# Optimization experiments

Measured on AMD Instinct MI355X. Metric: run time of the kernel, lower is better.

The kernel has to match this reference:

```python
import jax, jax.numpy as jnp
import numpy as np

HIDDEN = 2048
INTERMEDIATE = 8192
NUM_EXPERTS = 8
VOCAB = 100000
EXPERT_INTER = INTERMEDIATE // NUM_EXPERTS  # 1024
B, S = 4, 4096


def setup_inputs() -> dict:
    key = jax.random.key(0)
    k1, k2, k3, k4, k5 = jax.random.split(key, 5)
    hidden_states = jax.random.normal(k1, (B, S, HIDDEN), dtype=jnp.float32)
    token_ids = jax.random.randint(k2, (B, S), 0, VOCAB, dtype=jnp.int64)
    scale = 0.02
    gate_proj = jax.random.normal(k3, (NUM_EXPERTS, HIDDEN, EXPERT_INTER), dtype=jnp.float32) * scale
    up_proj = jax.random.normal(k4, (NUM_EXPERTS, HIDDEN, EXPERT_INTER), dtype=jnp.float32) * scale
    down_proj = jax.random.normal(k5, (NUM_EXPERTS, EXPERT_INTER, HIDDEN), dtype=jnp.float32) * scale
    return {
        "hidden_states": hidden_states,
        "token_ids": token_ids,
        "gate_proj": gate_proj,
        "up_proj": up_proj,
        "down_proj": down_proj,
    }


def _token_to_expert(token_ids):
    # Buffer in the torch module maps contiguous vocab buckets to experts;
    # remainder tokens go to the last expert.
    tokens_per_expert = VOCAB // NUM_EXPERTS
    ids = jnp.clip(token_ids, 0, VOCAB - 1)
    return jnp.minimum(ids // tokens_per_expert, NUM_EXPERTS - 1)


def reference(hidden_states, token_ids, gate_proj, up_proj, down_proj):
    batch, seq_len, hidden = hidden_states.shape
    expert_ids = _token_to_expert(token_ids).reshape(-1)  # [T]
    x = hidden_states.reshape(-1, hidden)  # [T, H]
    out = jnp.zeros_like(x)
    # Fixed small loop over experts (structurally distinct weight slices).
    # Masked dense compute is mathematically identical to the torch module's
    # sort -> per-expert GEMM -> scatter-back (the permutation cancels).
    for e in range(NUM_EXPERTS):
        mask = (expert_ids == e)[:, None]  # [T, 1]
        g = x @ gate_proj[e]               # [T, I_e]
        u = x @ up_proj[e]                 # [T, I_e]
        y = (jax.nn.silu(g) * u) @ down_proj[e]  # [T, H]
        out = out + jnp.where(mask, y, jnp.zeros((), dtype=y.dtype))
    return out.reshape(batch, seq_len, hidden)
```

## Files before the change

kernel.cpp:

```cpp
#include <hip/hip_runtime.h>
#include <hip/hip_bf16.h>
#include <cstdint>
#include <cstddef>

#define HIDDEN   2048
#define EINTER   1024
#define NEXP     8
#define VOCAB_SZ 100000
#define TOK_PER_EXP (VOCAB_SZ / NEXP)

typedef unsigned short u16;
typedef __attribute__((ext_vector_type(8))) short short8;
typedef __attribute__((ext_vector_type(4))) float floatx4;

__device__ __forceinline__ int expert_of(int id) {
  id = id < 0 ? 0 : (id > VOCAB_SZ - 1 ? VOCAB_SZ - 1 : id);
  int e = id / TOK_PER_EXP;
  return e > NEXP - 1 ? NEXP - 1 : e;
}

__global__ void count_kernel(const int* __restrict__ tok_ids, int* __restrict__ counts, int T) {
  int t = blockIdx.x * blockDim.x + threadIdx.x;
  if (t < T) atomicAdd(&counts[expert_of(tok_ids[t])], 1);
}

__global__ void scan_kernel(const int* __restrict__ counts, int* __restrict__ offsets,
                            int* __restrict__ cursors) {
  if (threadIdx.x == 0) {
    int s = 0;
    for (int e = 0; e < NEXP; ++e) { offsets[e] = s; cursors[e] = s; s += counts[e]; }
  }
}

__global__ void scatter_kernel(const int* __restrict__ tok_ids, int* __restrict__ cursors,
                               int* __restrict__ tok_list, int T) {
  int t = blockIdx.x * blockDim.x + threadIdx.x;
  if (t < T) {
    int e = expert_of(tok_ids[t]);
    int pos = atomicAdd(&cursors[e], 1);
    tok_list[pos] = t;
  }
}

__global__ void gather_x_kernel(const float* __restrict__ x, const int* __restrict__ tok_list,
                                u16* __restrict__ xp) {
  const int row = blockIdx.x;
  const int tok = tok_list[row];
  const float* src = x + (size_t)tok * HIDDEN;
  u16* dst = xp + (size_t)row * HIDDEN;
  const int k = threadIdx.x * 8;
  float4 a = *(const float4*)(src + k);
  float4 b = *(const float4*)(src + k + 4);
  union { uint4 u; u16 s[8]; } pk;
  const float f[8] = {a.x, a.y, a.z, a.w, b.x, b.y, b.z, b.w};
#pragma unroll
  for (int i = 0; i < 8; ++i) {
    __hip_bfloat16 h = __float2bfloat16(f[i]);
    pk.s[i] = *reinterpret_cast<u16*>(&h);
  }
  *(uint4*)(dst + k) = pk.u;
}

__global__ void transpose_cvt_kernel(const float* __restrict__ in, u16* __restrict__ outp,
                                     int R, int C) {
  __shared__ float ts[32][33];
  const size_t bo = (size_t)blockIdx.z * R * C;
  const int c0 = blockIdx.x * 32, r0 = blockIdx.y * 32;
  const int tc = threadIdx.x & 31, tr = threadIdx.x >> 5;
#pragma unroll
  for (int i = 0; i < 4; ++i) {
    int r = tr + i * 8;
    ts[r][tc] = in[bo + (size_t)(r0 + r) * C + c0 + tc];
  }
  __syncthreads();
#pragma unroll
  for (int i = 0; i < 4; ++i) {
    int c = tr + i * 8;
    __hip_bfloat16 h = __float2bfloat16(ts[tc][c]);
    outp[bo + (size_t)(c0 + c) * R + r0 + tc] = *reinterpret_cast<u16*>(&h);
  }
}

__global__ __launch_bounds__(256, 2) void gate_up_mfma(
    const u16* __restrict__ xp,
    const u16* __restrict__ Gt,
    const u16* __restrict__ Ut,
    const int* __restrict__ counts,
    const int* __restrict__ offsets,
    u16* __restrict__ act) {
  __shared__ __align__(16) u16 As[128][72];
  __shared__ __align__(16) u16 Bg[64][72];
  __shared__ __align__(16) u16 Bu[64][72];

  const int e = blockIdx.z;
  const int cnt = counts[e];
  const int row0 = blockIdx.y * 128;
  if (row0 >= cnt) return;
  const int off = offsets[e];
  const int i0 = blockIdx.x * 64;

  const int tid  = threadIdx.x;
  const int lane = tid & 63;
  const int wave = tid >> 6;
  const int quad = lane >> 4;
  const int l16  = lane & 15;

  const int arow = tid >> 3;
  const int ach  = tid & 7;

  const int wrow = (wave & 1) * 64;
  const int wcol = (wave >> 1) * 32;

  floatx4 accg[4][2], accu[4][2];
#pragma unroll
  for (int mf = 0; mf < 4; ++mf)
#pragma unroll
    for (int nf = 0; nf < 2; ++nf) {
      floatx4 z = {0.f, 0.f, 0.f, 0.f};
      accg[mf][nf] = z; accu[mf][nf] = z;
    }

  const u16* xbase = xp + (size_t)off * HIDDEN;
  const u16* gbase = Gt + ((size_t)e * EINTER + i0) * HIDDEN;
  const u16* ubase = Ut + ((size_t)e * EINTER + i0) * HIDDEN;

  for (int k0 = 0; k0 < HIDDEN; k0 += 64) {
#pragma unroll
    for (int it = 0; it < 4; ++it) {
      int r = arow + it * 32;
      int rg = row0 + r; rg = rg < cnt ? rg : cnt - 1;
      *(uint4*)&As[r][ach * 8] = *(const uint4*)(xbase + (size_t)rg * HIDDEN + k0 + ach * 8);
    }
#pragma unroll
    for (int it = 0; it < 2; ++it) {
      int n = arow + it * 32;
      *(uint4*)&Bg[n][ach * 8] = *(const uint4*)(gbase + (size_t)n * HIDDEN + k0 + ach * 8);
      *(uint4*)&Bu[n][ach * 8] = *(const uint4*)(ubase + (size_t)n * HIDDEN + k0 + ach * 8);
    }
    __syncthreads();
#pragma unroll
    for (int s = 0; s < 2; ++s) {
      short8 af[4], bgf[2], buf2[2];
#pragma unroll
      for (int mf = 0; mf < 4; ++mf)
        af[mf] = *(const short8*)&As[wrow + mf * 16 + l16][(s * 4 + quad) * 8];
#pragma unroll
      for (int nf = 0; nf < 2; ++nf) {
        bgf[nf]  = *(const short8*)&Bg[wcol + nf * 16 + l16][(s * 4 + quad) * 8];
        buf2[nf] = *(const short8*)&Bu[wcol + nf * 16 + l16][(s * 4 + quad) * 8];
      }
#pragma unroll
      for (int mf = 0; mf < 4; ++mf)
#pragma unroll
        for (int nf = 0; nf < 2; ++nf) {
          accg[mf][nf] = __builtin_amdgcn_mfma_f32_16x16x32_bf16(af[mf], bgf[nf],  accg[mf][nf], 0, 0, 0);
          accu[mf][nf] = __builtin_amdgcn_mfma_f32_16x16x32_bf16(af[mf], buf2[nf], accu[mf][nf], 0, 0, 0);
        }
    }
    __syncthreads();
  }

#pragma unroll
  for (int mf = 0; mf < 4; ++mf)
#pragma unroll
    for (int nf = 0; nf < 2; ++nf)
#pragma unroll
      for (int rg = 0; rg < 4; ++rg) {
        int r = wrow + mf * 16 + quad * 4 + rg;
        if (row0 + r < cnt) {
          float g = accg[mf][nf][rg];
          float u = accu[mf][nf][rg];
          float y = (g / (1.f + __expf(-g))) * u;
          __hip_bfloat16 h = __float2bfloat16(y);
          act[((size_t)(off + row0 + r)) * EINTER + i0 + wcol + nf * 16 + l16] =
              *reinterpret_cast<u16*>(&h);
        }
      }
}

__global__ __launch_bounds__(256, 2) void down_mfma(
    const u16* __restrict__ act,
    const u16* __restrict__ Dt,
    const int* __restrict__ counts,
    const int* __restrict__ offsets,
    const int* __restrict__ tok_list,
    float* __restrict__ out) {
  __shared__ __align__(16) u16 As[128][72];
  __shared__ __align__(16) u16 Bs[128][72];
  __shared__ int toks[128];

  const int e = blockIdx.z;
  const int cnt = counts[e];
  const int row0 = blockIdx.y * 128;
  if (row0 >= cnt) return;
  const int off = offsets[e];
  const int j0 = blockIdx.x * 128;

  const int tid  = threadIdx.x;
  const int lane = tid & 63;
  const int wave = tid >> 6;
  const int quad = lane >> 4;
  const int l16  = lane & 15;

  const int arow = tid >> 3;
  const int ach  = tid & 7;

  const int wrow = (wave & 1) * 64;
  const int wcol = (wave >> 1) * 64;

  if (tid < 128) {
    int r = row0 + tid;
    toks[tid] = tok_list[off + (r < cnt ? r : cnt - 1)];
  }

  floatx4 acc[4][4];
#pragma unroll
  for (int mf = 0; mf < 4; ++mf)
#pragma unroll
    for (int nf = 0; nf < 4; ++nf) {
      floatx4 z = {0.f, 0.f, 0.f, 0.f};
      acc[mf][nf] = z;
    }

  const u16* abase = act + (size_t)off * EINTER;
  const u16* dbase = Dt + ((size_t)e * HIDDEN + j0) * EINTER;

  for (int k0 = 0; k0 < EINTER; k0 += 64) {
#pragma unroll
    for (int it = 0; it < 4; ++it) {
      int r = arow + it * 32;
      int rg = row0 + r; rg = rg < cnt ? rg : cnt - 1;
      *(uint4*)&As[r][ach * 8] = *(const uint4*)(abase + (size_t)rg * EINTER + k0 + ach * 8);
    }
#pragma unroll
    for (int it = 0; it < 4; ++it) {
      int n = arow + it * 32;
      *(uint4*)&Bs[n][ach * 8] = *(const uint4*)(dbase + (size_t)n * EINTER + k0 + ach * 8);
    }
    __syncthreads();
#pragma unroll
    for (int s = 0; s < 2; ++s) {
      short8 af[4], bf[4];
#pragma unroll
      for (int mf = 0; mf < 4; ++mf)
        af[mf] = *(const short8*)&As[wrow + mf * 16 + l16][(s * 4 + quad) * 8];
#pragma unroll
      for (int nf = 0; nf < 4; ++nf)
        bf[nf] = *(const short8*)&Bs[wcol + nf * 16 + l16][(s * 4 + quad) * 8];
#pragma unroll
      for (int mf = 0; mf < 4; ++mf)
#pragma unroll
        for (int nf = 0; nf < 4; ++nf)
          acc[mf][nf] = __builtin_amdgcn_mfma_f32_16x16x32_bf16(af[mf], bf[nf], acc[mf][nf], 0, 0, 0);
    }
    __syncthreads();
  }

#pragma unroll
  for (int mf = 0; mf < 4; ++mf)
#pragma unroll
    for (int nf = 0; nf < 4; ++nf)
#pragma unroll
      for (int rg = 0; rg < 4; ++rg) {
        int r = wrow + mf * 16 + quad * 4 + rg;
        if (row0 + r < cnt)
          out[(size_t)toks[r] * HIDDEN + j0 + wcol + nf * 16 + l16] = acc[mf][nf][rg];
      }
}

#define TM 64
#define TN 64
#define TK 16

__global__ __launch_bounds__(256, 2) void gate_up_fp32(
    const float* __restrict__ x, const float* __restrict__ G, const float* __restrict__ U,
    const int* __restrict__ counts, const int* __restrict__ offsets,
    const int* __restrict__ tok_list, float* __restrict__ act) {
  __shared__ __align__(16) float Xs[TK][TM + 4];
  __shared__ __align__(16) float Gs[TK][TN];
  __shared__ __align__(16) float Us[TK][TN];
  __shared__ int toks[TM];
  const int e = blockIdx.z, cnt = counts[e], row0 = blockIdx.y * TM;
  if (row0 >= cnt) return;
  const int off = offsets[e], i0 = blockIdx.x * TN, tid = threadIdx.x;
  if (tid < TM) { int r = row0 + tid; toks[tid] = tok_list[off + (r < cnt ? r : 0)]; }
  __syncthreads();
  const float* Ge = G + (size_t)e * HIDDEN * EINTER + i0;
  const float* Ue = U + (size_t)e * HIDDEN * EINTER + i0;
  const int kk_ld = tid & 15, r_ld = tid >> 4, i_ld = tid & 63, k_ld = tid >> 6;
  const int tx = tid & 15, ty = tid >> 4;
  float ag[4][4] = {{0.f}}, au[4][4] = {{0.f}};
  for (int k0 = 0; k0 < HIDDEN; k0 += TK) {
#pragma unroll
    for (int rr = 0; rr < 4; ++rr) {
      int r = r_ld + rr * 16;
      Xs[kk_ld][r] = x[(size_t)toks[r] * HIDDEN + k0 + kk_ld];
    }
#pragma unroll
    for (int kk = 0; kk < 4; ++kk) {
      int k = k_ld + kk * 4;
      Gs[k][i_ld] = Ge[(size_t)(k0 + k) * EINTER + i_ld];
      Us[k][i_ld] = Ue[(size_t)(k0 + k) * EINTER + i_ld];
    }
    __syncthreads();
#pragma unroll
    for (int kk = 0; kk < TK; ++kk) {
      float4 a = *(const float4*)&Xs[kk][ty * 4];
      float4 bg = *(const float4*)&Gs[kk][tx * 4];
      float4 bu = *(const float4*)&Us[kk][tx * 4];
      const float av[4] = {a.x, a.y, a.z, a.w}, bgv[4] = {bg.x, bg.y, bg.z, bg.w},
                  buv[4] = {bu.x, bu.y, bu.z, bu.w};
#pragma unroll
      for (int i = 0; i < 4; ++i)
#pragma unroll
        for (int j = 0; j < 4; ++j) {
          ag[i][j] = fmaf(av[i], bgv[j], ag[i][j]);
          au[i][j] = fmaf(av[i], buv[j], au[i][j]);
        }
    }
    __syncthreads();
  }
#pragma unroll
  for (int i = 0; i < 4; ++i) {
    int r = row0 + ty * 4 + i;
    if (r < cnt) {
      float4 o; float* op = (float*)&o;
#pragma unroll
      for (int j = 0; j < 4; ++j) {
        float g = ag[i][j], u = au[i][j];
        op[j] = (g / (1.0f + expf(-g))) * u;
      }
      *(float4*)&act[(size_t)(off + r) * EINTER + i0 + tx * 4] = o;
    }
  }
}

__global__ __launch_bounds__(256, 2) void down_fp32(
    const float* __restrict__ act, const float* __restrict__ D,
    const int* __restrict__ counts, const int* __restrict__ offsets,
    const int* __restrict__ tok_list, float* __restrict__ out) {
  __shared__ __align__(16) float As[TK][TM + 4];
  __shared__ __align__(16) float Ds[TK][TN];
  __shared__ int toks[TM];
  const int e = blockIdx.z, cnt = counts[e], row0 = blockIdx.y * TM;
  if (row0 >= cnt) return;
  const int off = offsets[e], j0 = blockIdx.x * TN, tid = threadIdx.x;
  if (tid < TM) { int r = row0 + tid; toks[tid] = tok_list[off + (r < cnt ? r : 0)]; }
  const float* De = D + (size_t)e * EINTER * HIDDEN + j0;
  const int kk_ld = tid & 15, r_ld = tid >> 4, i_ld = tid & 63, k_ld = tid >> 6;
  const int tx = tid & 15, ty = tid >> 4;
  float acc[4][4] = {{0.f}};
  for (int k0 = 0; k0 < EINTER; k0 += TK) {
#pragma unroll
    for (int rr = 0; rr < 4; ++rr) {
      int r = r_ld + rr * 16;
      int grow = row0 + r;
      As[kk_ld][r] = act[(size_t)(off + (grow < cnt ? grow : 0)) * EINTER + k0 + kk_ld];
    }
#pragma unroll
    for (int kk = 0; kk < 4; ++kk) {
      int k = k_ld + kk * 4;
      Ds[k][i_ld] = De[(size_t)(k0 + k) * HIDDEN + i_ld];
    }
    __syncthreads();
#pragma unroll
    for (int kk = 0; kk < TK; ++kk) {
      float4 a = *(const float4*)&As[kk][ty * 4];
      float4 b = *(const float4*)&Ds[kk][tx * 4];
      const float av[4] = {a.x, a.y, a.z, a.w}, bv[4] = {b.x, b.y, b.z, b.w};
#pragma unroll
      for (int i = 0; i < 4; ++i)
#pragma unroll
        for (int j = 0; j < 4; ++j)
          acc[i][j] = fmaf(av[i], bv[j], acc[i][j]);
    }
    __syncthreads();
  }
#pragma unroll
  for (int i = 0; i < 4; ++i) {
    int r = row0 + ty * 4 + i;
    if (r < cnt) {
      float4 o = {acc[i][0], acc[i][1], acc[i][2], acc[i][3]};
      *(float4*)&out[(size_t)toks[ty * 4 + i] * HIDDEN + j0 + tx * 4] = o;
    }
  }
}

extern "C" void kernel_launch(void* const* d_in, const int* in_sizes, int n_in,
                              void* d_out, int out_size, void* d_ws, size_t ws_size,
                              hipStream_t stream) {
  const float* x       = (const float*)d_in[0];
  const int*   tok_ids = (const int*)d_in[1];
  const float* G       = (const float*)d_in[2];
  const float* U       = (const float*)d_in[3];
  const float* D       = (const float*)d_in[4];
  float* out = (float*)d_out;

  const int T = in_sizes[0] / HIDDEN;

  int* counts   = (int*)d_ws;
  int* offsets  = counts + NEXP;
  int* cursors  = offsets + NEXP;
  int* tok_list = cursors + NEXP;
  size_t hdr_bytes = (((size_t)(3 * NEXP + T) * sizeof(int)) + 255) & ~(size_t)255;

  hipMemsetAsync(counts, 0, NEXP * sizeof(int), stream);
  count_kernel<<<(T + 255) / 256, 256, 0, stream>>>(tok_ids, counts, T);
  scan_kernel<<<1, 64, 0, stream>>>(counts, offsets, cursors);
  scatter_kernel<<<(T + 255) / 256, 256, 0, stream>>>(tok_ids, cursors, tok_list, T);

  const size_t xp_bytes  = (size_t)T * HIDDEN * 2;
  const size_t w_bytes   = (size_t)NEXP * HIDDEN * EINTER * 2;
  const size_t act_bf16  = (size_t)T * EINTER * 2;
  const size_t need_bf16 = hdr_bytes + xp_bytes + 3 * w_bytes + act_bf16;

  if (ws_size >= need_bf16) {
    char* p = (char*)d_ws + hdr_bytes;
    u16* xp = (u16*)p;             p += xp_bytes;
    u16* Gt = (u16*)p;             p += w_bytes;
    u16* Ut = (u16*)p;             p += w_bytes;
    u16* Dt = (u16*)p;             p += w_bytes;
    u16* act = (u16*)p;

    gather_x_kernel<<<T, 256, 0, stream>>>(x, tok_list, xp);
    transpose_cvt_kernel<<<dim3(EINTER / 32, HIDDEN / 32, NEXP), 256, 0, stream>>>(G, Gt, HIDDEN, EINTER);
    transpose_cvt_kernel<<<dim3(EINTER / 32, HIDDEN / 32, NEXP), 256, 0, stream>>>(U, Ut, HIDDEN, EINTER);
    transpose_cvt_kernel<<<dim3(HIDDEN / 32, EINTER / 32, NEXP), 256, 0, stream>>>(D, Dt, EINTER, HIDDEN);

    dim3 g1(EINTER / 64, (T + 127) / 128, NEXP);
    gate_up_mfma<<<g1, 256, 0, stream>>>(xp, Gt, Ut, counts, offsets, act);
    dim3 g2(HIDDEN / 128, (T + 127) / 128, NEXP);
    down_mfma<<<g2, 256, 0, stream>>>(act, Dt, counts, offsets, tok_list, out);
  } else {
    float* act = (float*)((char*)d_ws + hdr_bytes);
    dim3 g1(EINTER / TN, (T + TM - 1) / TM, NEXP);
    gate_up_fp32<<<g1, 256, 0, stream>>>(x, G, U, counts, offsets, tok_list, act);
    dim3 g2(HIDDEN / TN, (T + TM - 1) / TM, NEXP);
    down_fp32<<<g2, 256, 0, stream>>>(act, D, counts, offsets, tok_list, out);
  }
}
```

Baseline: 855.5 us.

## Use direct global-to-LDS loads with XOR swizzle and widen weight transpose

Replaces register-staged global-to-shared tile copies in both MFMA GEMM kernels with global_load_lds 16-byte direct loads. The shared tiles drop their padding and use an XOR-swizzled chunk layout so fragment reads stay free of bank conflicts. The weight transpose/convert kernel moves to 64x64 tiles with float4 reads and 16-byte bf16 writes, and gate and up are handled in one launch. This cuts VGPR pressure and load instruction count in the GEMMs and improves transpose bandwidth, but relies on the direct-to-LDS path placing data exactly where the swizzle expects.

After: 740.4 us. 13.5% less time.

```diff
diff --git a/kernel.cpp b/kernel.cpp
--- a/kernel.cpp
+++ b/kernel.cpp
@@ -17,6 +17,16 @@
   id = id < 0 ? 0 : (id > VOCAB_SZ - 1 ? VOCAB_SZ - 1 : id);
   int e = id / TOK_PER_EXP;
   return e > NEXP - 1 ? NEXP - 1 : e;
+}
+
+__device__ __forceinline__ void gl16(const u16* g, u16* l) {
+  __builtin_amdgcn_global_load_lds(
+      (const __attribute__((address_space(1))) uint32_t*)g,
+      (__attribute__((address_space(3))) uint32_t*)l, 16, 0, 0);
+}
+
+__device__ __forceinline__ short8 ldfrag(const u16* base, int row, int chunk) {
+  return *(const short8*)(base + (row << 6) + (((chunk ^ (row & 7))) << 3));
 }
 
 __global__ void count_kernel(const int* __restrict__ tok_ids, int* __restrict__ counts, int T) {
@@ -61,36 +71,42 @@
   *(uint4*)(dst + k) = pk.u;
 }
 
-__global__ void transpose_cvt_kernel(const float* __restrict__ in, u16* __restrict__ outp,
-                                     int R, int C) {
-  __shared__ float ts[32][33];
-  const size_t bo = (size_t)blockIdx.z * R * C;
-  const int c0 = blockIdx.x * 32, r0 = blockIdx.y * 32;
-  const int tc = threadIdx.x & 31, tr = threadIdx.x >> 5;
-#pragma unroll
-  for (int i = 0; i < 4; ++i) {
-    int r = tr + i * 8;
-    ts[r][tc] = in[bo + (size_t)(r0 + r) * C + c0 + tc];
-  }
+__global__ void transpose_cvt64(const float* __restrict__ in0, u16* __restrict__ out0,
+                                const float* __restrict__ in1, u16* __restrict__ out1,
+                                int R, int C, int split) {
+  __shared__ float ts[64][65];
+  const int z = blockIdx.z;
+  const bool first = (z < split) || (in1 == nullptr);
+  const float* in = first ? in0 : in1;
+  u16* outp = first ? out0 : out1;
+  const int e = first ? z : z - split;
+  const size_t bo = (size_t)e * R * C;
+  const int c0 = blockIdx.x * 64, r0 = blockIdx.y * 64;
+  const int lr = threadIdx.x >> 2, lq = threadIdx.x & 3;
+#pragma unroll
+  for (int j = 0; j < 4; ++j)
+    *(float4*)&ts[lr][lq * 16 + j * 4] =
+        *(const float4*)&in[bo + (size_t)(r0 + lr) * C + c0 + lq * 16 + j * 4];
   __syncthreads();
 #pragma unroll
-  for (int i = 0; i < 4; ++i) {
-    int c = tr + i * 8;
-    __hip_bfloat16 h = __float2bfloat16(ts[tc][c]);
-    outp[bo + (size_t)(c0 + c) * R + r0 + tc] = *reinterpret_cast<u16*>(&h);
+  for (int j = 0; j < 2; ++j) {
+    union { uint4 u; u16 s[8]; } pk;
+#pragma unroll
+    for (int i = 0; i < 8; ++i) {
+      __hip_bfloat16 h = __float2bfloat16(ts[lq * 16 + j * 8 + i][lr]);
+      pk.s[i] = *reinterpret_cast<u16*>(&h);
+    }
+    *(uint4*)&outp[bo + (size_t)(c0 + lr) * R + r0 + lq * 16 + j * 8] = pk.u;
   }
 }
 
 __global__ __launch_bounds__(256, 2) void gate_up_mfma(
-    const u16* __restrict__ xp,
-    const u16* __restrict__ Gt,
-    const u16* __restrict__ Ut,
-    const int* __restrict__ counts,
-    const int* __restrict__ offsets,
+    const u16* __restrict__ xp, const u16* __restrict__ Gt, const u16* __restrict__ Ut,
+    const int* __restrict__ counts, const int* __restrict__ offsets,
     u16* __restrict__ act) {
-  __shared__ __align__(16) u16 As[128][72];
-  __shared__ __align__(16) u16 Bg[64][72];
-  __shared__ __align__(16) u16 Bu[64][72];
+  __shared__ __align__(16) u16 As[128 * 64];
+  __shared__ __align__(16) u16 Bg[64 * 64];
+  __shared__ __align__(16) u16 Bu[64 * 64];
 
   const int e = blockIdx.z;
   const int cnt = counts[e];
@@ -105,11 +121,27 @@
   const int quad = lane >> 4;
   const int l16  = lane & 15;
 
-  const int arow = tid >> 3;
-  const int ach  = tid & 7;
+  const int lrow   = lane >> 3;
+  const int lchunk = (lane & 7) ^ lrow;
 
   const int wrow = (wave & 1) * 64;
   const int wcol = (wave >> 1) * 32;
+
+  const u16* aptr[4];
+#pragma unroll
+  for (int it = 0; it < 4; ++it) {
+    int r = ((wave + 4 * it) << 3) + lrow;
+    int rg = row0 + r; rg = rg < cnt ? rg : cnt - 1;
+    aptr[it] = xp + (size_t)(off + rg) * HIDDEN + (lchunk << 3);
+  }
+  const u16* gptr[2];
+  const u16* uptr[2];
+#pragma unroll
+  for (int it = 0; it < 2; ++it) {
+    int n = ((wave + 4 * it) << 3) + lrow;
+    gptr[it] = Gt + ((size_t)e * EINTER + i0 + n) * HIDDEN + (lchunk << 3);
+    uptr[it] = Ut + ((size_t)e * EINTER + i0 + n) * HIDDEN + (lchunk << 3);
+  }
 
   floatx4 accg[4][2], accu[4][2];
 #pragma unroll
@@ -120,22 +152,14 @@
       accg[mf][nf] = z; accu[mf][nf] = z;
     }
 
-  const u16* xbase = xp + (size_t)off * HIDDEN;
-  const u16* gbase = Gt + ((size_t)e * EINTER + i0) * HIDDEN;
-  const u16* ubase = Ut + ((size_t)e * EINTER + i0) * HIDDEN;
-
   for (int k0 = 0; k0 < HIDDEN; k0 += 64) {
 #pragma unroll
-    for (int it = 0; it < 4; ++it) {
-      int r = arow + it * 32;
-      int rg = row0 + r; rg = rg < cnt ? rg : cnt - 1;
-      *(uint4*)&As[r][ach * 8] = *(const uint4*)(xbase + (size_t)rg * HIDDEN + k0 + ach * 8);
-    }
+    for (int it = 0; it < 4; ++it)
+      gl16(aptr[it] + k0, &As[(wave + 4 * it) << 9]);
 #pragma unroll
     for (int it = 0; it < 2; ++it) {
-      int n = arow + it * 32;
-      *(uint4*)&Bg[n][ach * 8] = *(const uint4*)(gbase + (size_t)n * HIDDEN + k0 + ach * 8);
-      *(uint4*)&Bu[n][ach * 8] = *(const uint4*)(ubase + (size_t)n * HIDDEN + k0 + ach * 8);
+      gl16(gptr[it] + k0, &Bg[(wave + 4 * it) << 9]);
+      gl16(uptr[it] + k0, &Bu[(wave + 4 * it) << 9]);
     }
     __syncthreads();
 #pragma unroll
@@ -143,11 +167,11 @@
       short8 af[4], bgf[2], buf2[2];
 #pragma unroll
       for (int mf = 0; mf < 4; ++mf)
-        af[mf] = *(const short8*)&As[wrow + mf * 16 + l16][(s * 4 + quad) * 8];
+        af[mf] = ldfrag(As, wrow + mf * 16 + l16, s * 4 + quad);
 #pragma unroll
       for (int nf = 0; nf < 2; ++nf) {
-        bgf[nf]  = *(const short8*)&Bg[wcol + nf * 16 + l16][(s * 4 + quad) * 8];
-        buf2[nf] = *(const short8*)&Bu[wcol + nf * 16 + l16][(s * 4 + quad) * 8];
+        bgf[nf]  = ldfrag(Bg, wcol + nf * 16 + l16, s * 4 + quad);
+        buf2[nf] = ldfrag(Bu, wcol + nf * 16 + l16, s * 4 + quad);
       }
 #pragma unroll
       for (int mf = 0; mf < 4; ++mf)
@@ -179,14 +203,11 @@
 }
 
 __global__ __launch_bounds__(256, 2) void down_mfma(
-    const u16* __restrict__ act,
-    const u16* __restrict__ Dt,
-    const int* __restrict__ counts,
-    const int* __restrict__ offsets,
-    const int* __restrict__ tok_list,
-    float* __restrict__ out) {
-  __shared__ __align__(16) u16 As[128][72];
-  __shared__ __align__(16) u16 Bs[128][72];
+    const u16* __restrict__ act, const u16* __restrict__ Dt,
+    const int* __restrict__ counts, const int* __restrict__ offsets,
+    const int* __restrict__ tok_list, float* __restrict__ out) {
+  __shared__ __align__(16) u16 As[128 * 64];
+  __shared__ __align__(16) u16 Bs[128 * 64];
   __shared__ int toks[128];
 
   const int e = blockIdx.z;
@@ -202,8 +223,8 @@
   const int quad = lane >> 4;
   const int l16  = lane & 15;
 
-  const int arow = tid >> 3;
-  const int ach  = tid & 7;
+  const int lrow   = lane >> 3;
+  const int lchunk = (lane & 7) ^ lrow;
 
   const int wrow = (wave & 1) * 64;
   const int wcol = (wave >> 1) * 64;
@@ -213,6 +234,16 @@
     toks[tid] = tok_list[off + (r < cnt ? r : cnt - 1)];
   }
 
+  const u16* aptr[4];
+  const u16* dptr[4];
+#pragma unroll
+  for (int it = 0; it < 4; ++it) {
+    int r = ((wave + 4 * it) << 3) + lrow;
+    int rg = row0 + r; rg = rg < cnt ? rg : cnt - 1;
+    aptr[it] = act + (size_t)(off + rg) * EINTER + (lchunk << 3);
+    dptr[it] = Dt + ((size_t)e * HIDDEN + j0 + r) * EINTER + (lchunk << 3);
+  }
+
   floatx4 acc[4][4];
 #pragma unroll
   for (int mf = 0; mf < 4; ++mf)
@@ -222,20 +253,11 @@
       acc[mf][nf] = z;
     }
 
-  const u16* abase = act + (size_t)off * EINTER;
-  const u16* dbase = Dt + ((size_t)e * HIDDEN + j0) * EINTER;
-
   for (int k0 = 0; k0 < EINTER; k0 += 64) {
 #pragma unroll
     for (int it = 0; it < 4; ++it) {
-      int r = arow + it * 32;
-      int rg = row0 + r; rg = rg < cnt ? rg : cnt - 1;
-      *(uint4*)&As[r][ach * 8] = *(const uint4*)(abase + (size_t)rg * EINTER + k0 + ach * 8);
-    }
-#pragma unroll
-    for (int it = 0; it < 4; ++it) {
-      int n = arow + it * 32;
-      *(uint4*)&Bs[n][ach * 8] = *(const uint4*)(dbase + (size_t)n * EINTER + k0 + ach * 8);
+      gl16(aptr[it] + k0, &As[(wave + 4 * it) << 9]);
+      gl16(dptr[it] + k0, &Bs[(wave + 4 * it) << 9]);
     }
     __syncthreads();
 #pragma unroll
@@ -243,10 +265,10 @@
       short8 af[4], bf[4];
 #pragma unroll
       for (int mf = 0; mf < 4; ++mf)
-        af[mf] = *(const short8*)&As[wrow + mf * 16 + l16][(s * 4 + quad) * 8];
+        af[mf] = ldfrag(As, wrow + mf * 16 + l16, s * 4 + quad);
 #pragma unroll
       for (int nf = 0; nf < 4; ++nf)
-        bf[nf] = *(const short8*)&Bs[wcol + nf * 16 + l16][(s * 4 + quad) * 8];
+        bf[nf] = ldfrag(Bs, wcol + nf * 16 + l16, s * 4 + quad);
 #pragma unroll
       for (int mf = 0; mf < 4; ++mf)
 #pragma unroll
@@ -416,16 +438,17 @@
 
   if (ws_size >= need_bf16) {
     char* p = (char*)d_ws + hdr_bytes;
-    u16* xp = (u16*)p;             p += xp_bytes;
-    u16* Gt = (u16*)p;             p += w_bytes;
-    u16* Ut = (u16*)p;             p += w_bytes;
-    u16* Dt = (u16*)p;             p += w_bytes;
+    u16* xp = (u16*)p;   p += xp_bytes;
+    u16* Gt = (u16*)p;   p += w_bytes;
+    u16* Ut = (u16*)p;   p += w_bytes;
+    u16* Dt = (u16*)p;   p += w_bytes;
     u16* act = (u16*)p;
 
     gather_x_kernel<<<T, 256, 0, stream>>>(x, tok_list, xp);
-    transpose_cvt_kernel<<<dim3(EINTER / 32, HIDDEN / 32, NEXP), 256, 0, stream>>>(G, Gt, HIDDEN, EINTER);
-    transpose_cvt_kernel<<<dim3(EINTER / 32, HIDDEN / 32, NEXP), 256, 0, stream>>>(U, Ut, HIDDEN, EINTER);
-    transpose_cvt_kernel<<<dim3(HIDDEN / 32, EINTER / 32, NEXP), 256, 0, stream>>>(D, Dt, EINTER, HIDDEN);
+    transpose_cvt64<<<dim3(EINTER / 64, HIDDEN / 64, 2 * NEXP), 256, 0, stream>>>(
+        G, Gt, U, Ut, HIDDEN, EINTER, NEXP);
+    transpose_cvt64<<<dim3(HIDDEN / 64, EINTER / 64, NEXP), 256, 0, stream>>>(
+        D, Dt, nullptr, nullptr, EINTER, HIDDEN, NEXP);
 
     dim3 g1(EINTER / 64, (T + 127) / 128, NEXP);
     gate_up_mfma<<<g1, 256, 0, stream>>>(xp, Gt, Ut, counts, offsets, act);
```
